# Kernel tuning notes

Measured on AMD Instinct MI355X. Metric: run time of the kernel, lower is better.

The kernel has to match this reference:

```python
import jax, jax.numpy as jnp
import numpy as np

B, L, H, N2, NLAYERS = 8, 4096, 256, 32, 4


def setup_inputs() -> dict:
    key = jax.random.key(0)
    ks = jax.random.split(key, 7)
    x = jax.random.normal(ks[0], (B, L, H), dtype=jnp.float32)
    # S4D kernel params (per layer, stacked on leading dim)
    dt_min, dt_max = 1e-3, 1e-1
    u = jax.random.uniform(ks[1], (NLAYERS, H), dtype=jnp.float32)
    log_dt = u * (np.log(dt_max) - np.log(dt_min)) + np.log(dt_min)
    log_A_real = jnp.log(0.5 * jnp.ones((NLAYERS, H, N2), jnp.float32))
    A_imag = jnp.broadcast_to(np.pi * jnp.arange(N2, dtype=jnp.float32), (NLAYERS, H, N2)) * jnp.ones((NLAYERS, H, N2), jnp.float32)
    C_re = jax.random.normal(ks[2], (NLAYERS, H, N2), dtype=jnp.float32) * (0.5 ** 0.5)
    C_im = jax.random.normal(ks[3], (NLAYERS, H, N2), dtype=jnp.float32) * (0.5 ** 0.5)
    D = jax.random.normal(ks[4], (NLAYERS, H), dtype=jnp.float32)
    Wout = jax.random.normal(ks[5], (NLAYERS, 2 * H, H), dtype=jnp.float32) * (1.0 / H) ** 0.5
    bout = jnp.zeros((NLAYERS, 2 * H), jnp.float32)
    ln_g = jnp.ones((NLAYERS, H), jnp.float32)
    ln_b = jnp.zeros((NLAYERS, H), jnp.float32)
    return dict(x=x, log_dt=log_dt, log_A_real=log_A_real, A_imag=A_imag,
                C_re=C_re, C_im=C_im, D=D, Wout=Wout, bout=bout,
                ln_g=ln_g, ln_b=ln_b)


def _s4d_kernel(log_dt, log_A_real, A_imag, C_re, C_im, Lseq):
    # Vandermonde kernel of S4D: k[h,l] = 2*Re sum_n C'_hn exp(dt_h*A_hn*l)
    dt = jnp.exp(log_dt)                       # (H,)
    A = (-jnp.exp(log_A_real) + 1j * A_imag)   # (H,N) complex
    C = C_re + 1j * C_im                       # (H,N)
    dtA = A * dt[:, None]                      # (H,N)
    K = jnp.exp(dtA[:, :, None] * jnp.arange(Lseq, dtype=jnp.float32))  # (H,N,L)
    Cm = C * (jnp.exp(dtA) - 1.0) / A          # ZOH discretization of C
    return 2.0 * jnp.einsum('hn,hnl->hl', Cm, K).real  # (H,L)


def _s4d_layer(u, log_dt, log_A_real, A_imag, C_re, C_im, D, Wout, bout):
    # u: (B,H,L)
    Lq = u.shape[-1]
    k = _s4d_kernel(log_dt, log_A_real, A_imag, C_re, C_im, Lq)  # (H,L)
    kf = jnp.fft.rfft(k, n=2 * Lq)             # (H, L+1)
    uf = jnp.fft.rfft(u, n=2 * Lq)             # (B,H,L+1)
    y = jnp.fft.irfft(uf * kf, n=2 * Lq)[..., :Lq]
    y = y + u * D[:, None]
    y = jax.nn.gelu(y, approximate=False)
    # output linear: 1x1 conv H->2H followed by GLU along channel dim
    y = jnp.einsum('oh,bhl->bol', Wout, y) + bout[None, :, None]
    a, b = jnp.split(y, 2, axis=1)
    return a * jax.nn.sigmoid(b)               # (B,H,L)


def _layernorm_ch(x, g, b, eps=1e-5):
    # x: (B,H,L); normalize over channel axis H (matches norm on (B,L,H))
    m = jnp.mean(x, axis=1, keepdims=True)
    v = jnp.mean((x - m) ** 2, axis=1, keepdims=True)
    return (x - m) / jnp.sqrt(v + eps) * g[None, :, None] + b[None, :, None]


def reference(x, log_dt, log_A_real, A_imag, C_re, C_im, D, Wout, bout, ln_g, ln_b):
    u = jnp.swapaxes(x, -1, -2)  # (B,H,L)
    for i in range(NLAYERS):  # post-norm (prenorm=False), dropout=identity (eval)
        z = _s4d_layer(u, log_dt[i], log_A_real[i], A_imag[i], C_re[i], C_im[i],
                       D[i], Wout[i], bout[i])
        u = z + u
        u = _layernorm_ch(u, ln_g[i], ln_b[i])
    return jnp.swapaxes(u, -1, -2)  # (B,L,H)
```

## Files before the change

### kernel.cpp

```cpp
#include <hip/hip_runtime.h>
#include <math.h>

#define B    8
#define L    4096
#define H    256
#define N2   32
#define NL   4
#define O2   512
#define BLK  64
#define NBLK 64
#define TVP  136
#define MJP  72
#define UTP  72
#define INP  68
#define TL2  64
#define YPAD 264

typedef __attribute__((ext_vector_type(8))) short short8;
typedef __attribute__((ext_vector_type(4))) float f32x4;

__device__ __forceinline__ unsigned short f2bf(float f)
{
    unsigned int u = __float_as_uint(f);
    unsigned int r = (u + 0x7fffu + ((u >> 16) & 1u)) >> 16;
    return (unsigned short)r;
}

__device__ __forceinline__ float bf2f(unsigned short v)
{
    return __uint_as_float(((unsigned int)v) << 16);
}

__device__ __forceinline__ float gelu_f(float x)
{
    float t = 1.59576912161f * fmaf(0.044715f * x * x, x, x);
    return x / (1.f + __expf(-t));
}

__global__ __launch_bounds__(256) void k_setup(
    const float* __restrict__ x, const float* __restrict__ log_dt,
    const float* __restrict__ log_Ar, const float* __restrict__ A_im,
    const float* __restrict__ C_re, const float* __restrict__ C_im,
    const float* __restrict__ Dv, const float* __restrict__ Wout,
    unsigned short* __restrict__ Wb, unsigned short* __restrict__ TVc,
    unsigned short* __restrict__ Mm, float2* __restrict__ w64c,
    unsigned short* __restrict__ u)
{
    __shared__ float sh[32 * 33];
    const int bid = blockIdx.x;
    const int t = threadIdx.x;

    if (bid < 512) {
        int idx = (bid * 256 + t) * 4;
        float4 v = *(const float4*)(Wout + idx);
        ushort4 o;
        o.x = f2bf(v.x); o.y = f2bf(v.y); o.z = f2bf(v.z); o.w = f2bf(v.w);
        *(ushort4*)(Wb + idx) = o;
    } else if (bid < 640) {
        float* kb = sh;
        const int g = t >> 5, n = t & 31;
        const int id = (bid - 512) * 8 + g;
        const int layer = id >> 8, h = id & 255;
        const int idx = (layer * H + h) * N2 + n;
        double dt = exp((double)log_dt[layer * H + h]);
        double Ar = -exp((double)log_Ar[idx]);
        double Ai = (double)A_im[idx];
        double dtr = dt * Ar, dti = dt * Ai;
        double er = exp(dtr);
        double dwr = er * cos(dti), dwi = er * sin(dti);
        double numr = dwr - 1.0, numi = dwi;
        double den = Ar * Ar + Ai * Ai;
        double qr0 = (numr * Ar + numi * Ai) / den;
        double qi0 = (numi * Ar - numr * Ai) / den;
        double dcr = (double)C_re[idx], dci = (double)C_im[idx];
        const float wr = (float)dwr, wi = (float)dwi;
        const float cr = (float)(2.0 * (dcr * qr0 - dci * qi0));
        const float ci = (float)(2.0 * (dcr * qi0 + dci * qr0));
        const float Dh = Dv[layer * H + h];
        unsigned short* tv = TVc + (size_t)(layer * H + h) * BLK * TVP;
        unsigned short* mm = Mm + (size_t)(layer * H + h) * BLK * MJP;
        float vr = 1.f, vi = 0.f;
        for (int d = 0; d < BLK; ++d) {
            float pk = fmaf(cr, vr, -(ci * vi));
            pk += __shfl_xor(pk, 1);  pk += __shfl_xor(pk, 2);
            pk += __shfl_xor(pk, 4);  pk += __shfl_xor(pk, 8);
            pk += __shfl_xor(pk, 16);
            if (n == 0) kb[g * 64 + d] = pk;
            mm[n * MJP + (63 - d)]        = f2bf(vr);
            mm[(32 + n) * MJP + (63 - d)] = f2bf(vi);
            float nvr = vr * wr - vi * wi;
            float nvi = vr * wi + vi * wr;
            vr = nvr; vi = nvi;
            float qr = fmaf(cr, vr, -(ci * vi));
            float qi = fmaf(cr, vi, ci * vr);
            tv[d * TVP + 64 + n] = f2bf(qr);
            tv[d * TVP + 96 + n] = f2bf(-qi);
        }
        w64c[(layer * H + h) * N2 + n] = make_float2(vr, vi);
        __syncthreads();
        for (int i = 0; i < BLK; ++i) {
#pragma unroll
            for (int hf = 0; hf < 2; ++hf) {
                int j = n + hf * 32;
                float val = (j > i) ? 0.f : ((j == i) ? (kb[g * 64] + Dh) : kb[g * 64 + i - j]);
                tv[i * TVP + j] = f2bf(val);
            }
        }
    } else {
        float (*tt)[33] = (float(*)[33])sh;
        const int rb = bid - 640;
        const int hx = rb & 7, ly = (rb >> 3) & 127, b = rb >> 10;
        const int h0 = hx * 32, l0 = ly * 32;
        const int tx = t & 31, ty = t >> 5;
        const float* xb = x + (size_t)b * L * H;
        unsigned short* ub = u + (size_t)b * H * L;
#pragma unroll
        for (int i = 0; i < 4; ++i)
            tt[ty + i * 8][tx] = xb[(size_t)(l0 + ty + i * 8) * H + h0 + tx];
        __syncthreads();
#pragma unroll
        for (int i = 0; i < 4; ++i)
            ub[(size_t)(h0 + ty + i * 8) * L + l0 + tx] = f2bf(tt[tx][ty + i * 8]);
    }
}

__global__ __launch_bounds__(256) void k_scan3(
    const unsigned short* __restrict__ u, const unsigned short* __restrict__ Mm_l,
    const unsigned short* __restrict__ TVc_l, const float2* __restrict__ w64c_l,
    unsigned short* __restrict__ y)
{
    __shared__ __align__(16) unsigned short uT[BLK * UTP];
    __shared__ __align__(16) unsigned short ST[BLK * UTP];
    __shared__ __align__(16) float INC[BLK * INP];
    __shared__ float2 cLd[4][32];
    const int t = threadIdx.x;
    const int wv = t >> 6, lane = t & 63;
    const int lanei = lane & 15, quad = lane >> 4;
    const int h = blockIdx.x >> 3, ct = blockIdx.x & 7;
    const unsigned short* ub = u + (size_t)(ct * H + h) * L;

    {
        int col = t >> 2, q = t & 3;
        *(short8*)&uT[col * UTP + q * 16]     = *(const short8*)(ub + col * 64 + q * 16);
        *(short8*)&uT[col * UTP + q * 16 + 8] = *(const short8*)(ub + col * 64 + q * 16 + 8);
    }
    __syncthreads();

    {
        f32x4 acc[4];
#pragma unroll
        for (int nt = 0; nt < 4; ++nt) acc[nt] = (f32x4){0.f, 0.f, 0.f, 0.f};
        const unsigned short* bcol = &uT[(wv * 16 + lanei) * UTP + quad * 8];
        const unsigned short* abase = Mm_l + (size_t)h * BLK * MJP + lanei * MJP + quad * 8;
#pragma unroll
        for (int kt = 0; kt < 2; ++kt) {
            short8 b8 = *(const short8*)(bcol + kt * 32);
#pragma unroll
            for (int nt = 0; nt < 4; ++nt) {
                short8 a8 = *(const short8*)(abase + (nt * 16) * MJP + kt * 32);
                acc[nt] = __builtin_amdgcn_mfma_f32_16x16x32_bf16(a8, b8, acc[nt], 0, 0, 0);
            }
        }
#pragma unroll
        for (int nt = 0; nt < 4; ++nt)
            *(f32x4*)&INC[(wv * 16 + lanei) * INP + nt * 16 + quad * 4] = acc[nt];
    }

    const int n = lane & 31;
    float Pr[16], Pi[16];
    float w1r = 1.f, w1i = 0.f;
    float2 w64 = make_float2(0.f, 0.f);
    if (lane < 32) {
        w64 = w64c_l[h * N2 + n];
        float sr = 0.f, si = 0.f;
        const int base = wv * 16;
#pragma unroll
        for (int k = 0; k < 16; ++k) {
            Pr[k] = sr; Pi[k] = si;
            float ir = INC[(base + k) * INP + n];
            float ii = INC[(base + k) * INP + 32 + n];
            float nr = fmaf(w64.x, sr, fmaf(-w64.y, si, ir));
            float ni = fmaf(w64.x, si, fmaf(w64.y, sr, ii));
            sr = nr; si = ni;
        }
        cLd[wv][n] = make_float2(sr, si);
        float ar = w64.x, ai = w64.y;
#pragma unroll
        for (int q = 0; q < 4; ++q) {
            float nr2 = ar * ar - ai * ai;
            float ni2 = 2.f * ar * ai;
            ar = nr2; ai = ni2;
        }
        w1r = ar; w1i = ai;
    }
    __syncthreads();
    if (lane < 32) {
        float Cr = 0.f, Ci = 0.f;
        for (int wp = 0; wp < wv; ++wp) {
            float2 Lw = cLd[wp][n];
            float nr = fmaf(w1r, Cr, fmaf(-w1i, Ci, Lw.x));
            float ni = fmaf(w1r, Ci, fmaf(w1i, Cr, Lw.y));
            Cr = nr; Ci = ni;
        }
        float pr = 1.f, pi = 0.f;
#pragma unroll
        for (int k = 0; k < 16; ++k) {
            int blk = wv * 16 + k;
            float Sr = fmaf(pr, Cr, fmaf(-pi, Ci, Pr[k]));
            float Si = fmaf(pr, Ci, fmaf(pi, Cr, Pi[k]));
            ST[blk * UTP + n]      = f2bf(Sr);
            ST[blk * UTP + 32 + n] = f2bf(Si);
            float npr = pr * w64.x - pi * w64.y;
            float npi = pr * w64.y + pi * w64.x;
            pr = npr; pi = npi;
        }
    }

    {
        f32x4 acc[4];
#pragma unroll
        for (int nt = 0; nt < 4; ++nt) acc[nt] = (f32x4){0.f, 0.f, 0.f, 0.f};
        const unsigned short* abase = TVc_l + (size_t)h * BLK * TVP + lanei * TVP + quad * 8;
#pragma unroll
        for (int kt = 0; kt < 4; ++kt) {
            const unsigned short* bb = (kt < 2) ? uT : ST;
            short8 b8 = *(const short8*)&bb[(wv * 16 + lanei) * UTP + (kt & 1) * 32 + quad * 8];
#pragma unroll
            for (int nt = 0; nt < 4; ++nt) {
                short8 a8 = *(const short8*)(abase + (nt * 16) * TVP + kt * 32);
                acc[nt] = __builtin_amdgcn_mfma_f32_16x16x32_bf16(a8, b8, acc[nt], 0, 0, 0);
            }
        }
        unsigned short* yb = y + (size_t)(ct * H + h) * L;
#pragma unroll
        for (int nt = 0; nt < 4; ++nt) {
            int blk = wv * 16 + lanei;
            int i0 = nt * 16 + quad * 4;
            ushort4 o4;
            o4.x = f2bf(gelu_f(acc[nt][0]));
            o4.y = f2bf(gelu_f(acc[nt][1]));
            o4.z = f2bf(gelu_f(acc[nt][2]));
            o4.w = f2bf(gelu_f(acc[nt][3]));
            *(ushort4*)(yb + blk * 64 + i0) = o4;
        }
    }
}

__global__ __launch_bounds__(512, 4) void k_gemm(
    const unsigned short* __restrict__ y, unsigned short* __restrict__ u,
    const unsigned short* __restrict__ Wb, const float* __restrict__ bo,
    const float* __restrict__ lng, const float* __restrict__ lnb,
    float* __restrict__ outp)
{
    __shared__ __align__(16) unsigned short yS[TL2 * YPAD];
    __shared__ float bS[O2];
    __shared__ float lgS[H], lbS[H];
    __shared__ float redS[8][4][16], redQ[8][4][16];

    const int t = threadIdx.x;
    const int wv = t >> 6;
    const int lane = t & 63;
    const int lanei = lane & 15;
    const int quad = lane >> 4;
    const int b = blockIdx.x >> 6;
    const int l0 = (blockIdx.x & 63) * TL2;

    size_t abase[2][2];
#pragma unroll
    for (int p = 0; p < 2; ++p)
#pragma unroll
        for (int jj = 0; jj < 2; ++jj)
            abase[p][jj] = (size_t)(p * 256 + wv * 32 + jj * 16 + lanei) * H + quad * 8;

    short8 a8p[4];
#pragma unroll
    for (int p = 0; p < 2; ++p)
#pragma unroll
        for (int jj = 0; jj < 2; ++jj)
            a8p[p * 2 + jj] = *(const short8*)(Wb + abase[p][jj]);

    {
        const int i = t & 7, hr = t >> 3;
        const unsigned short* yb = y + (size_t)b * H * L + l0 + i * 8;
#pragma unroll
        for (int ps = 0; ps < 4; ++ps) {
            int h = ps * 64 + hr;
            short8 v8 = *(const short8*)(yb + (size_t)h * L);
#pragma unroll
            for (int r = 0; r < 8; ++r)
                yS[(i * 8 + r) * YPAD + (h ^ (8 * i))] = (unsigned short)v8[r];
        }
        if (t < O2) bS[t] = bo[t];
        if (t < H) { lgS[t] = lng[t]; lbS[t] = lnb[t]; }
    }
    __syncthreads();

    f32x4 acc[2][2][4];
#pragma unroll
    for (int p = 0; p < 2; ++p)
#pragma unroll
        for (int jj = 0; jj < 2; ++jj)
#pragma unroll
            for (int nt = 0; nt < 4; ++nt)
                acc[p][jj][nt] = (f32x4){0.f, 0.f, 0.f, 0.f};

#pragma unroll
    for (int kt = 0; kt < 8; ++kt) {
        short8 bfr[4];
#pragma unroll
        for (int nt = 0; nt < 4; ++nt) {
            int lp = nt * 16 + lanei;
            int a = (2 * nt + (lanei >> 3)) & 7;
            bfr[nt] = *(const short8*)&yS[lp * YPAD + ((kt * 32 + quad * 8) ^ (8 * a))];
        }
#pragma unroll
        for (int p = 0; p < 2; ++p)
#pragma unroll
            for (int jj = 0; jj < 2; ++jj) {
                short8 a8 = (kt == 0) ? a8p[p * 2 + jj]
                                      : *(const short8*)(Wb + abase[p][jj] + kt * 32);
#pragma unroll
                for (int nt = 0; nt < 4; ++nt)
                    acc[p][jj][nt] = __builtin_amdgcn_mfma_f32_16x16x32_bf16(
                        a8, bfr[nt], acc[p][jj][nt], 0, 0, 0);
            }
    }

    float psum[4] = {0.f, 0.f, 0.f, 0.f}, psq[4] = {0.f, 0.f, 0.f, 0.f};
    unsigned short* ub = u + (size_t)b * H * L + l0;
#pragma unroll
    for (int jj = 0; jj < 2; ++jj) {
#pragma unroll
        for (int nt = 0; nt < 4; ++nt) {
            int lc = nt * 16 + lanei;
#pragma unroll
            for (int reg = 0; reg < 4; ++reg) {
                int o = wv * 32 + jj * 16 + quad * 4 + reg;
                float a = acc[0][jj][nt][reg] + bS[o];
                float g = acc[1][jj][nt][reg] + bS[o + 256];
                float glu = a / (1.f + __expf(-g));
                float val = glu + bf2f(ub[(size_t)o * L + lc]);
                acc[0][jj][nt][reg] = val;
                psum[nt] += val;
                psq[nt] = fmaf(val, val, psq[nt]);
            }
        }
    }
#pragma unroll
    for (int nt = 0; nt < 4; ++nt) {
        psum[nt] += __shfl_xor(psum[nt], 16);
        psum[nt] += __shfl_xor(psum[nt], 32);
        psq[nt]  += __shfl_xor(psq[nt], 16);
        psq[nt]  += __shfl_xor(psq[nt], 32);
    }
    if (lane < 16) {
#pragma unroll
        for (int nt = 0; nt < 4; ++nt) {
            redS[wv][nt][lanei] = psum[nt];
            redQ[wv][nt][lanei] = psq[nt];
        }
    }
    __syncthreads();
    float mcol[4], icol[4];
#pragma unroll
    for (int nt = 0; nt < 4; ++nt) {
        float s = 0.f, q = 0.f;
#pragma unroll
        for (int w = 0; w < 8; ++w) { s += redS[w][nt][lanei]; q += redQ[w][nt][lanei]; }
        float m = s * (1.0f / 256.0f);
        float v = q * (1.0f / 256.0f) - m * m;
        mcol[nt] = m;
        icol[nt] = rsqrtf(v + 1e-5f);
    }
    if (outp == nullptr) {
#pragma unroll
        for (int jj = 0; jj < 2; ++jj) {
#pragma unroll
            for (int nt = 0; nt < 4; ++nt) {
                int lc = nt * 16 + lanei;
#pragma unroll
                for (int reg = 0; reg < 4; ++reg) {
                    int o = wv * 32 + jj * 16 + quad * 4 + reg;
                    float val = acc[0][jj][nt][reg];
                    float ov = (val - mcol[nt]) * icol[nt] * lgS[o] + lbS[o];
                    ub[(size_t)o * L + lc] = f2bf(ov);
                }
            }
        }
    } else {
#pragma unroll
        for (int jj = 0; jj < 2; ++jj) {
#pragma unroll
            for (int nt = 0; nt < 4; ++nt) {
                int lc = nt * 16 + lanei;
                int o0 = wv * 32 + jj * 16 + quad * 4;
                float4 ov;
#pragma unroll
                for (int reg = 0; reg < 4; ++reg) {
                    int o = o0 + reg;
                    float val = acc[0][jj][nt][reg];
                    ((float*)&ov)[reg] = (val - mcol[nt]) * icol[nt] * lgS[o] + lbS[o];
                }
                *(float4*)(outp + ((size_t)b * L + l0 + lc) * H + o0) = ov;
            }
        }
    }
}

extern "C" void kernel_launch(void* const* d_in, const int* in_sizes, int n_in,
                              void* d_out, int out_size, void* d_ws, size_t ws_size,
                              hipStream_t stream)
{
    const float* x      = (const float*)d_in[0];
    const float* log_dt = (const float*)d_in[1];
    const float* log_Ar = (const float*)d_in[2];
    const float* A_im   = (const float*)d_in[3];
    const float* C_re   = (const float*)d_in[4];
    const float* C_im   = (const float*)d_in[5];
    const float* Dv     = (const float*)d_in[6];
    const float* Wout   = (const float*)d_in[7];
    const float* bout   = (const float*)d_in[8];
    const float* lng    = (const float*)d_in[9];
    const float* lnb    = (const float*)d_in[10];
    float* out = (float*)d_out;

    unsigned short* u   = (unsigned short*)d_ws;
    unsigned short* Wb  = u + (size_t)B * H * L;
    unsigned short* TVc = Wb + (size_t)NL * O2 * H;
    unsigned short* Mm  = TVc + (size_t)NL * H * BLK * TVP;
    float2* w64c        = (float2*)(Mm + (size_t)NL * H * BLK * MJP);
    unsigned short* y   = (unsigned short*)(w64c + (size_t)NL * H * N2);

    k_setup<<<8832, 256, 0, stream>>>(x, log_dt, log_Ar, A_im, C_re, C_im, Dv, Wout,
                                      Wb, TVc, Mm, w64c, u);
    for (int layer = 0; layer < NL; ++layer) {
        k_scan3<<<H * 8, 256, 0, stream>>>(u, Mm + (size_t)layer * H * BLK * MJP,
                                           TVc + (size_t)layer * H * BLK * TVP,
                                           w64c + (size_t)layer * H * N2, y);
        k_gemm<<<B * L / TL2, 512, 0, stream>>>(y, u, Wb + (size_t)layer * O2 * H,
                                                bout + layer * O2, lng + layer * H, lnb + layer * H,
                                                (layer == NL - 1) ? out : nullptr);
    }
}
```

Before: 326.4 us.

## Vectorize input transpose tiles and swap MFMA operand roles in scan kernel

The input transpose in k_setup now handles 64x32 tiles, using float4 global loads and 16-byte bf16 stores, which halves the number of transpose blocks. In k_scan3 both MFMA stages now hold the per-channel matrix (Mm/TVc) row fragment in registers and stream the block data from LDS, instead of re-reading global matrix fragments for each output tile. This cuts global/L2 reads of the matrices. Output index mapping changes to match, and explicit __syncthreads are added around the INC/ST shared buffers, since rows are now written by different waves.

```diff
diff --git a/kernel.cpp b/kernel.cpp
--- a/kernel.cpp
+++ b/kernel.cpp
@@ -46,7 +46,7 @@
     unsigned short* __restrict__ Mm, float2* __restrict__ w64c,
     unsigned short* __restrict__ u)
 {
-    __shared__ float sh[32 * 33];
+    __shared__ float sh[32 * 68];
     const int bid = blockIdx.x;
     const int t = threadIdx.x;
 
@@ -107,20 +107,27 @@
             }
         }
     } else {
-        float (*tt)[33] = (float(*)[33])sh;
         const int rb = bid - 640;
-        const int hx = rb & 7, ly = (rb >> 3) & 127, b = rb >> 10;
-        const int h0 = hx * 32, l0 = ly * 32;
-        const int tx = t & 31, ty = t >> 5;
-        const float* xb = x + (size_t)b * L * H;
-        unsigned short* ub = u + (size_t)b * H * L;
-#pragma unroll
-        for (int i = 0; i < 4; ++i)
-            tt[ty + i * 8][tx] = xb[(size_t)(l0 + ty + i * 8) * H + h0 + tx];
+        const int hx = rb & 7, ly = (rb >> 3) & 63, b = rb >> 9;
+        const int h0 = hx * 32, l0 = ly * 64;
+        const int tx = t & 7, ty = t >> 3;
+        const float* xb = x + ((size_t)b * L + l0) * H + h0;
+#pragma unroll
+        for (int i = 0; i < 2; ++i) {
+            int l = ty + i * 32;
+            float4 v = *(const float4*)(xb + (size_t)l * H + tx * 4);
+            sh[(tx * 4 + 0) * 68 + l] = v.x;
+            sh[(tx * 4 + 1) * 68 + l] = v.y;
+            sh[(tx * 4 + 2) * 68 + l] = v.z;
+            sh[(tx * 4 + 3) * 68 + l] = v.w;
+        }
         __syncthreads();
-#pragma unroll
-        for (int i = 0; i < 4; ++i)
-            ub[(size_t)(h0 + ty + i * 8) * L + l0 + tx] = f2bf(tt[tx][ty + i * 8]);
+        const int hh = t >> 3, cc = (t & 7) * 8;
+        const float* row = &sh[hh * 68 + cc];
+        short8 o8;
+#pragma unroll
+        for (int j = 0; j < 8; ++j) o8[j] = (short)f2bf(row[j]);
+        *(short8*)(u + ((size_t)b * H + h0 + hh) * L + l0 + cc) = o8;
     }
 }
 
@@ -150,21 +157,21 @@
         f32x4 acc[4];
 #pragma unroll
         for (int nt = 0; nt < 4; ++nt) acc[nt] = (f32x4){0.f, 0.f, 0.f, 0.f};
-        const unsigned short* bcol = &uT[(wv * 16 + lanei) * UTP + quad * 8];
-        const unsigned short* abase = Mm_l + (size_t)h * BLK * MJP + lanei * MJP + quad * 8;
+        const unsigned short* arow = Mm_l + (size_t)h * BLK * MJP + (wv * 16 + lanei) * MJP + quad * 8;
 #pragma unroll
         for (int kt = 0; kt < 2; ++kt) {
-            short8 b8 = *(const short8*)(bcol + kt * 32);
+            short8 a8 = *(const short8*)(arow + kt * 32);
 #pragma unroll
             for (int nt = 0; nt < 4; ++nt) {
-                short8 a8 = *(const short8*)(abase + (nt * 16) * MJP + kt * 32);
+                short8 b8 = *(const short8*)&uT[(nt * 16 + lanei) * UTP + kt * 32 + quad * 8];
                 acc[nt] = __builtin_amdgcn_mfma_f32_16x16x32_bf16(a8, b8, acc[nt], 0, 0, 0);
             }
         }
 #pragma unroll
         for (int nt = 0; nt < 4; ++nt)
-            *(f32x4*)&INC[(wv * 16 + lanei) * INP + nt * 16 + quad * 4] = acc[nt];
-    }
+            *(f32x4*)&INC[(nt * 16 + lanei) * INP + wv * 16 + quad * 4] = acc[nt];
+    }
+    __syncthreads();
 
     const int n = lane & 31;
     float Pr[16], Pi[16];
@@ -215,27 +222,29 @@
             pr = npr; pi = npi;
         }
     }
+    __syncthreads();
 
     {
         f32x4 acc[4];
 #pragma unroll
         for (int nt = 0; nt < 4; ++nt) acc[nt] = (f32x4){0.f, 0.f, 0.f, 0.f};
-        const unsigned short* abase = TVc_l + (size_t)h * BLK * TVP + lanei * TVP + quad * 8;
+        const unsigned short* arow = TVc_l + (size_t)h * BLK * TVP + (wv * 16 + lanei) * TVP + quad * 8;
 #pragma unroll
         for (int kt = 0; kt < 4; ++kt) {
+            short8 a8 = *(const short8*)(arow + kt * 32);
             const unsigned short* bb = (kt < 2) ? uT : ST;
-            short8 b8 = *(const short8*)&bb[(wv * 16 + lanei) * UTP + (kt & 1) * 32 + quad * 8];
+            int ko = (kt & 1) * 32 + quad * 8;
 #pragma unroll
             for (int nt = 0; nt < 4; ++nt) {
-                short8 a8 = *(const short8*)(abase + (nt * 16) * TVP + kt * 32);
+                short8 b8 = *(const short8*)&bb[(nt * 16 + lanei) * UTP + ko];
                 acc[nt] = __builtin_amdgcn_mfma_f32_16x16x32_bf16(a8, b8, acc[nt], 0, 0, 0);
             }
         }
         unsigned short* yb = y + (size_t)(ct * H + h) * L;
 #pragma unroll
         for (int nt = 0; nt < 4; ++nt) {
-            int blk = wv * 16 + lanei;
-            int i0 = nt * 16 + quad * 4;
+            int blk = nt * 16 + lanei;
+            int i0 = wv * 16 + quad * 4;
             ushort4 o4;
             o4.x = f2bf(gelu_f(acc[nt][0]));
             o4.y = f2bf(gelu_f(acc[nt][1]));
@@ -431,7 +440,7 @@
     float2* w64c        = (float2*)(Mm + (size_t)NL * H * BLK * MJP);
     unsigned short* y   = (unsigned short*)(w64c + (size_t)NL * H * N2);
 
-    k_setup<<<8832, 256, 0, stream>>>(x, log_dt, log_Ar, A_im, C_re, C_im, Dv, Wout,
+    k_setup<<<4736, 256, 0, stream>>>(x, log_dt, log_Ar, A_im, C_re, C_im, Dv, Wout,
                                       Wb, TVc, Mm, w64c, u);
     for (int layer = 0; layer < NL; ++layer) {
         k_scan3<<<H * 8, 256, 0, stream>>>(u, Mm + (size_t)layer * H * BLK * MJP,
```

Result: faster. 314.6 us (-3.6%).
